# Kernel tuning notes

Measured on AMD Instinct MI355X. Metric: run time of the kernel, lower is better.

## Reference

```python
import jax, jax.numpy as jnp
import numpy as np

H, C = 8, 16          # heads, per-head dim; hidden = H*C = 128
NEG_SLOPE = 0.2       # GATConv default
EPS = 1e-5            # GraphNorm eps


def setup_inputs() -> dict:
    key = jax.random.key(0)
    ks = iter(jax.random.split(key, 64))
    Np, Na, D, E = 100000, 50000, 128, 500000
    s = 1.0 / np.sqrt(D)

    def w(shape, scale=1.0):
        return jax.random.normal(next(ks), shape, jnp.float32) * scale

    inp = {
        'x_paper': w((Np, D)),
        'x_author': w((Na, D)),
        'edge_writes': jnp.stack([
            jax.random.randint(next(ks), (E,), 0, Na),
            jax.random.randint(next(ks), (E,), 0, Np)]).astype(jnp.int32),
        'edge_cites': jnp.stack([
            jax.random.randint(next(ks), (E,), 0, Np),
            jax.random.randint(next(ks), (E,), 0, Np)]).astype(jnp.int32),
        'W_lin_paper': w((D, 128), s), 'b_lin_paper': jnp.zeros((128,), jnp.float32),
        'W_lin_author': w((D, 128), s), 'b_lin_author': jnp.zeros((128,), jnp.float32),
        'Wsrc_writes': w((128, 128), s), 'Wdst_writes': w((128, 128), s),
        'atts_writes': w((H, C), 0.1), 'attd_writes': w((H, C), 0.1),
        'bias_writes': jnp.zeros((128,), jnp.float32),
        'Wsrc_cites': w((128, 128), s), 'Wdst_cites': w((128, 128), s),
        'atts_cites': w((H, C), 0.1), 'attd_cites': w((H, C), 0.1),
        'bias_cites': jnp.zeros((128,), jnp.float32),
        'gnw_paper': jnp.ones((128,), jnp.float32), 'gnb_paper': jnp.zeros((128,), jnp.float32),
        'gnm_paper': jnp.ones((128,), jnp.float32),
        'gnw_author': jnp.ones((128,), jnp.float32), 'gnb_author': jnp.zeros((128,), jnp.float32),
        'gnm_author': jnp.ones((128,), jnp.float32),
        'W2_paper': w((128, 128), s), 'b2_paper': jnp.zeros((128,), jnp.float32),
        'W2_author': w((128, 128), s), 'b2_author': jnp.zeros((128,), jnp.float32),
    }
    return inp


def _gat(src_emb, dst_emb, ei, Wsrc, Wdst, att_s, att_d, bias, n_dst):
    # PyG GATConv, bipartite input, concat=True, add_self_loops=True (eval / no dropout)
    n_self = min(src_emb.shape[0], n_dst)
    loops = jnp.arange(n_self, dtype=ei.dtype)
    src = jnp.concatenate([ei[0], loops])
    dst = jnp.concatenate([ei[1], loops])
    xs = (src_emb @ Wsrc).reshape(-1, H, C)          # [Ns,H,C]
    xd = (dst_emb @ Wdst).reshape(-1, H, C)          # [Nd,H,C]
    a_s = (xs * att_s).sum(-1)                       # [Ns,H]
    a_d = (xd * att_d).sum(-1)                       # [Nd,H]
    e = jax.nn.leaky_relu(a_s[src] + a_d[dst], NEG_SLOPE)   # [E,H]
    m = jax.ops.segment_max(e, dst, num_segments=n_dst)
    m = jnp.where(jnp.isfinite(m), m, 0.0)           # guard empty segments
    p = jnp.exp(e - m[dst])
    denom = jax.ops.segment_sum(p, dst, num_segments=n_dst)
    alpha = p / (denom[dst] + 1e-16)                 # segment softmax over dst
    msg = xs[src] * alpha[:, :, None]                # [E,H,C]
    out = jax.ops.segment_sum(msg, dst, num_segments=n_dst)  # [Nd,H,C]
    return out.reshape(n_dst, H * C) + bias


def _gnorm(x, w, b, ms):
    mu = x.mean(0)
    o = x - ms * mu
    var = (o * o).mean(0)
    return w * o * jax.lax.rsqrt(var + EPS) + b


def reference(x_paper, x_author, edge_writes, edge_cites,
              W_lin_paper, b_lin_paper, W_lin_author, b_lin_author,
              Wsrc_writes, Wdst_writes, atts_writes, attd_writes, bias_writes,
              Wsrc_cites, Wdst_cites, atts_cites, attd_cites, bias_cites,
              gnw_paper, gnb_paper, gnm_paper, gnw_author, gnb_author, gnm_author,
              W2_paper, b2_paper, W2_author, b2_author):
    emb_p = jax.nn.relu(x_paper @ W_lin_paper + b_lin_paper)
    emb_a = jax.nn.relu(x_author @ W_lin_author + b_lin_author)
    Np = emb_p.shape[0]
    out_p = _gat(emb_a, emb_p, edge_writes, Wsrc_writes, Wdst_writes,
                 atts_writes, attd_writes, bias_writes, Np)
    out_p = out_p + _gat(emb_p, emb_p, edge_cites, Wsrc_cites, Wdst_cites,
                         atts_cites, attd_cites, bias_cites, Np)
    out_a = jnp.zeros((emb_a.shape[0], H * C), x_author.dtype)  # no edge type targets author
    out_p = _gnorm(out_p, gnw_paper, gnb_paper, gnm_paper) @ W2_paper + b2_paper
    out_a = _gnorm(out_a, gnw_author, gnb_author, gnm_author) @ W2_author + b2_author
    return (out_p, out_a)
```

## Files before the change

kernel.cpp:

```cpp
#include <hip/hip_runtime.h>
#include <cstdint>
#include <cstddef>

#define H 8
#define DHID 128
#define BM 64
#define LDST 136
#define NEG_SLOPE 0.2f
#define GN_EPS 1e-5f

#define SCAN_T 256
#define SCAN_I 4

typedef __attribute__((ext_vector_type(8))) short short8;
typedef __attribute__((ext_vector_type(4))) float f32x4;

__device__ __forceinline__ void atomAddF(float* p, float v) {
    __hip_atomic_fetch_add(p, v, __ATOMIC_RELAXED, __HIP_MEMORY_SCOPE_AGENT);
}
__device__ __forceinline__ unsigned short f2bf(float f) {
    uint32_t u = __float_as_uint(f);
    uint32_t r = (u + 0x7FFFu + ((u >> 16) & 1u)) >> 16;
    return (unsigned short)r;
}
__device__ __forceinline__ uint32_t pack2bf(float lo, float hi) {
    return (uint32_t)f2bf(lo) | ((uint32_t)f2bf(hi) << 16);
}
__device__ __forceinline__ float bflo(uint32_t v) { return __uint_as_float(v << 16); }
__device__ __forceinline__ float bfhi(uint32_t v) { return __uint_as_float(v & 0xFFFF0000u); }

struct PrepHist {
    const float *Wlp, *Wsc, *Wla, *Wsw, *W2p;
    const float *Wdw, *adw, *asc_, *Wdc, *adc_, *asw_;
    unsigned short *WlinP_p, *WsrcP_c, *WlinP_a, *WsrcP_w, *W2P_p, *VscP_p, *VscP_a;
    const float *bw, *bc, *gnb_a, *W2a, *b2a;
    float *bsum, *row_a, *colsum, *colsumsq;
    unsigned short *xs_w_ph, *xs_c_ph;
    float *as_w_ph, *as_c_ph;
    const int *dst_w, *dst_c;
    int *deg, *rank;
    int Ew, Ec, Np, HB0;
};

__global__ void prep_hist(PrepHist a) {
    int b = blockIdx.x, t = threadIdx.x;
    if (b >= a.HB0) {
        int base = (b - a.HB0) * 1024 + t;
        int E = a.Ew + a.Ec;
        int dd[4];
        bool val[4];
#pragma unroll
        for (int j = 0; j < 4; ++j) {
            int i = base + j * 256;
            val[j] = i < E;
            dd[j] = 0;
            if (val[j]) dd[j] = (i < a.Ew) ? a.dst_w[i] : (a.Np + a.dst_c[i - a.Ew]);
        }
        int rk[4];
#pragma unroll
        for (int j = 0; j < 4; ++j)
            if (val[j]) rk[j] = atomicAdd(&a.deg[dd[j]], 1);
#pragma unroll
        for (int j = 0; j < 4; ++j)
            if (val[j]) a.rank[base + j * 256] = rk[j];
        return;
    }
    if (b == 56) {
        if (t < 128) {
            a.bsum[t] = a.bw[t] + a.bc[t];
            float acc = a.b2a[t];
            for (int k = 0; k < DHID; ++k) acc += a.gnb_a[k] * a.W2a[k * DHID + t];
            a.row_a[t] = acc;
            a.colsum[t] = 0.f;
            a.colsumsq[t] = 0.f;
            a.xs_w_ph[t] = 0;
            a.xs_c_ph[t] = 0;
        } else if (t < 136) a.as_w_ph[t - 128] = -1e30f;
        else if (t < 144) a.as_c_ph[t - 136] = -1e30f;
        return;
    }
    int j = b >> 3;
    int idx = (b & 7) * 256 + t;
    int lane = idx & 63, kk = (idx >> 6) & 3, nt = idx >> 8;
    int col = nt * 16 + (lane & 15);
    int k0 = kk * 32 + ((lane >> 4) << 3);
    if (j < 5) {
        const float* W = j == 0 ? a.Wlp : j == 1 ? a.Wsc : j == 2 ? a.Wla : j == 3 ? a.Wsw : a.W2p;
        unsigned short* out = j == 0 ? a.WlinP_p : j == 1 ? a.WsrcP_c : j == 2 ? a.WlinP_a
                              : j == 3 ? a.WsrcP_w : a.W2P_p;
        for (int i = 0; i < 8; ++i) out[idx * 8 + i] = f2bf(W[(k0 + i) * DHID + col]);
    } else if (j == 5) {
        if (idx >= 2 * 256) return;
        const float *W = nullptr, *A = nullptr;
        int h = col & 7;
        if (col < 24) {
            int which = col >> 3;
            W = which == 0 ? a.Wdw : which == 1 ? a.Wsc : a.Wdc;
            A = which == 0 ? a.adw : which == 1 ? a.asc_ : a.adc_;
        }
        for (int i = 0; i < 8; ++i) {
            float v = 0.f;
            if (W)
                for (int c = 0; c < 16; ++c) v += W[(k0 + i) * DHID + h * 16 + c] * A[h * 16 + c];
            a.VscP_p[idx * 8 + i] = f2bf(v);
        }
    } else {
        if (idx >= 256) return;
        int h = col & 7;
        for (int i = 0; i < 8; ++i) {
            float v = 0.f;
            if (col < 8)
                for (int c = 0; c < 16; ++c)
                    v += a.Wsw[(k0 + i) * DHID + h * 16 + c] * a.asw_[h * 16 + c];
            a.VscP_a[idx * 8 + i] = f2bf(v);
        }
    }
}

__global__ void scan1(const int* __restrict__ in, int n, int* __restrict__ out,
                      int* __restrict__ bsums) {
    __shared__ int sh[SCAN_T];
    int t = threadIdx.x;
    long base = (long)blockIdx.x * SCAN_T * SCAN_I;
    int v[SCAN_I];
    int s = 0;
#pragma unroll
    for (int j = 0; j < SCAN_I; ++j) {
        long idx = base + (long)t * SCAN_I + j;
        int x = (idx < n) ? in[idx] : 0;
        x = (x + 3) & ~3;
        v[j] = x;
        s += x;
    }
    sh[t] = s;
    __syncthreads();
    for (int off = 1; off < SCAN_T; off <<= 1) {
        int x = (t >= off) ? sh[t - off] : 0;
        __syncthreads();
        sh[t] += x;
        __syncthreads();
    }
    int run = sh[t] - s;
#pragma unroll
    for (int j = 0; j < SCAN_I; ++j) {
        long idx = base + (long)t * SCAN_I + j;
        if (idx < n) out[idx] = run;
        run += v[j];
    }
    if (t == SCAN_T - 1) bsums[blockIdx.x] = sh[SCAN_T - 1];
}

__global__ void scan3_tails(const int* __restrict__ off_raw, const int* __restrict__ bs1,
                            int nb, int n2, int* __restrict__ off2,
                            const int* __restrict__ deg,
                            int Np, int Na, int* __restrict__ srcu) {
    __shared__ int pf[SCAN_T];
    int t = threadIdx.x;
    pf[t] = (t < nb) ? bs1[t] : 0;
    __syncthreads();
    for (int off = 1; off < SCAN_T; off <<= 1) {
        int x = (t >= off) ? pf[t - off] : 0;
        __syncthreads();
        pf[t] += x;
        __syncthreads();
    }
    int i = blockIdx.x * 256 + t;
    if (i < n2) {
        int g = i >> 10;
        int o = off_raw[i] + (g ? pf[g - 1] : 0);
        off2[i] = o;
        int dgi = deg[i];
        int padded = (dgi + 3) & ~3;
        int ph = (i < Np) ? Na : Np;
        for (int k = dgi; k < padded; ++k) srcu[o + k] = ph;
    }
    if (blockIdx.x == 0 && t == 0) off2[n2] = pf[nb - 1];
}

template <int NSC>
__device__ void proj_body(unsigned short* xt, int bid,
                          const float* __restrict__ x, int nrows,
                          const unsigned short* __restrict__ WlinP, const float* __restrict__ blin,
                          const unsigned short* __restrict__ WsrcP,
                          const unsigned short* __restrict__ VscP,
                          unsigned short* __restrict__ xs,
                          float* __restrict__ a0, float* __restrict__ a1, float* __restrict__ a2) {
    int t = threadIdx.x;
    int lane = t & 63, w = t >> 6;
    long row0 = (long)bid * BM;
    int wrow0 = w * 16;
    for (int it = 0; it < 16; ++it) {
        int r = wrow0 + it;
        long gr = row0 + r;
        float v0 = 0.f, v1 = 0.f;
        if (gr < nrows) { v0 = x[gr * DHID + 2 * lane]; v1 = x[gr * DHID + 2 * lane + 1]; }
        *reinterpret_cast<uint32_t*>(&xt[r * LDST + 2 * lane]) = pack2bf(v0, v1);
    }
    int arow = wrow0 + (lane & 15);
    int koff = (lane >> 4) << 3;
    short8 af[4];
#pragma unroll
    for (int kk = 0; kk < 4; ++kk)
        af[kk] = *reinterpret_cast<const short8*>(&xt[arow * LDST + kk * 32 + koff]);
    const short8* Bl = reinterpret_cast<const short8*>(WlinP);
    f32x4 acc[8];
#pragma unroll
    for (int nt = 0; nt < 8; ++nt) {
        f32x4 a = {0.f, 0.f, 0.f, 0.f};
#pragma unroll
        for (int kk = 0; kk < 4; ++kk)
            a = __builtin_amdgcn_mfma_f32_16x16x32_bf16(af[kk], Bl[(nt * 4 + kk) * 64 + lane], a, 0, 0, 0);
        acc[nt] = a;
    }
    int orow = wrow0 + ((lane >> 4) << 2);
    int ccol = lane & 15;
#pragma unroll
    for (int nt = 0; nt < 8; ++nt) {
        float b = blin[nt * 16 + ccol];
#pragma unroll
        for (int r = 0; r < 4; ++r) {
            float e = fmaxf(acc[nt][r] + b, 0.f);
            xt[(orow + r) * LDST + nt * 16 + ccol] = f2bf(e);
        }
    }
#pragma unroll
    for (int kk = 0; kk < 4; ++kk)
        af[kk] = *reinterpret_cast<const short8*>(&xt[arow * LDST + kk * 32 + koff]);
    const short8* Bs = reinterpret_cast<const short8*>(WsrcP);
#pragma unroll
    for (int nt = 0; nt < 8; ++nt) {
        f32x4 a = {0.f, 0.f, 0.f, 0.f};
#pragma unroll
        for (int kk = 0; kk < 4; ++kk)
            a = __builtin_amdgcn_mfma_f32_16x16x32_bf16(af[kk], Bs[(nt * 4 + kk) * 64 + lane], a, 0, 0, 0);
        acc[nt] = a;
    }
    const short8* Bv = reinterpret_cast<const short8*>(VscP);
    f32x4 sacc0 = {0.f, 0.f, 0.f, 0.f}, sacc1 = {0.f, 0.f, 0.f, 0.f};
#pragma unroll
    for (int kk = 0; kk < 4; ++kk)
        sacc0 = __builtin_amdgcn_mfma_f32_16x16x32_bf16(af[kk], Bv[kk * 64 + lane], sacc0, 0, 0, 0);
    if (NSC > 1) {
#pragma unroll
        for (int kk = 0; kk < 4; ++kk)
            sacc1 = __builtin_amdgcn_mfma_f32_16x16x32_bf16(af[kk], Bv[(4 + kk) * 64 + lane], sacc1, 0, 0, 0);
    }
#pragma unroll
    for (int nt = 0; nt < 8; ++nt) {
#pragma unroll
        for (int r = 0; r < 4; ++r) {
            long gr = row0 + orow + r;
            if (gr < nrows) xs[gr * DHID + nt * 16 + ccol] = f2bf(acc[nt][r]);
        }
    }
#pragma unroll
    for (int st = 0; st < NSC; ++st) {
        int scol = st * 16 + ccol;
        int h = scol & 7, which = scol >> 3;
        float* ap = which == 0 ? a0 : which == 1 ? a1 : which == 2 ? a2 : nullptr;
        if (ap) {
            f32x4 s = st == 0 ? sacc0 : sacc1;
#pragma unroll
            for (int r = 0; r < 4; ++r) {
                long gr = row0 + orow + r;
                if (gr < nrows) ap[gr * H + h] = s[r];
            }
        }
    }
}

struct MegaArgs {
    const float* x_p; int Np;
    const unsigned short* WlinP_p; const float* blp;
    const unsigned short* WsrcP_c; const unsigned short* VscP_p;
    unsigned short* xs_c; float *a_d_w, *a_s_c, *a_d_c;
    const float* x_a; int Na;
    const unsigned short* WlinP_a; const float* bla;
    const unsigned short* WsrcP_w; const unsigned short* VscP_a;
    unsigned short* xs_w; float* a_s_w;
    const int *src_w, *dst_w, *src_c, *dst_c;
    int Ew, Ec;
    const int *off2, *rank;
    int* srcu;
    int PB, AB;
};

__global__ __launch_bounds__(256) void mega(MegaArgs a) {
    __shared__ unsigned short xt[BM * LDST];
    int b = blockIdx.x;
    if (b < a.PB) {
        proj_body<2>(xt, b, a.x_p, a.Np, a.WlinP_p, a.blp, a.WsrcP_c, a.VscP_p,
                     a.xs_c, a.a_d_w, a.a_s_c, a.a_d_c);
        return;
    }
    if (b < a.PB + a.AB) {
        proj_body<1>(xt, b - a.PB, a.x_a, a.Na, a.WlinP_a, a.bla, a.WsrcP_w, a.VscP_a,
                     a.xs_w, a.a_s_w, nullptr, nullptr);
        return;
    }
    int base = (b - a.PB - a.AB) * 1024 + threadIdx.x;
    int E = a.Ew + a.Ec;
    int s[4], di[4], rk[4];
    bool val[4];
#pragma unroll
    for (int j = 0; j < 4; ++j) {
        int i = base + j * 256;
        val[j] = i < E;
        s[j] = di[j] = rk[j] = 0;
        if (val[j]) {
            if (i < a.Ew) { s[j] = a.src_w[i]; di[j] = a.dst_w[i]; }
            else { int q = i - a.Ew; s[j] = a.src_c[q]; di[j] = a.Np + a.dst_c[q]; }
            rk[j] = a.rank[i];
        }
    }
    int pos[4];
#pragma unroll
    for (int j = 0; j < 4; ++j)
        if (val[j]) pos[j] = a.off2[di[j]] + rk[j];
#pragma unroll
    for (int j = 0; j < 4; ++j)
        if (val[j]) a.srcu[pos[j]] = s[j];
}

#define FILLB 391
__global__ __launch_bounds__(256) void gat_gather(
    const int* __restrict__ off, const int* __restrict__ srcu,
    const float* __restrict__ a_s_w, const float* __restrict__ a_d_w,
    const float* __restrict__ a_s_c, const float* __restrict__ a_d_c,
    const unsigned short* __restrict__ xs_w, const unsigned short* __restrict__ xs_c,
    uint32_t* __restrict__ gatb, int Np, int nselfw,
    const float* __restrict__ row_a, float4* __restrict__ outa, long n4) {
    if (blockIdx.x < FILLB) {
        long i = (long)blockIdx.x * 256 + threadIdx.x;
        long stride = (long)FILLB * 256;
        const float4* r4 = reinterpret_cast<const float4*>(row_a);
        for (; i < n4; i += stride) outa[i] = r4[i & 31];
        return;
    }
    int l = threadIdx.x & 63;
    int d = (blockIdx.x - FILLB) * 4 + (threadIdx.x >> 6);
    if (d >= Np) return;
    int h = l >> 3;
    int iw = off[d], w1 = off[d + 1];
    int ic = off[Np + d], c1 = off[Np + d + 1];
    float adw = a_d_w[(long)d * H + h];
    float adc = a_d_c[(long)d * H + h];
    float denw = 0.f, n0w = 0.f, n1w = 0.f;
    float denc = 0.f, n0c = 0.f, n1c = 0.f;
    if (d < nselfw) {
        float e = a_s_w[(long)d * H + h] + adw;
        e = e > 0.f ? e : NEG_SLOPE * e;
        float p = __expf(e);
        uint32_t v = *reinterpret_cast<const uint32_t*>(xs_w + (long)d * DHID + 2 * l);
        denw += p; n0w += p * bflo(v); n1w += p * bfhi(v);
    }
    {
        float e = a_s_c[(long)d * H + h] + adc;
        e = e > 0.f ? e : NEG_SLOPE * e;
        float p = __expf(e);
        uint32_t v = *reinterpret_cast<const uint32_t*>(xs_c + (long)d * DHID + 2 * l);
        denc += p; n0c += p * bflo(v); n1c += p * bfhi(v);
    }
    while (iw < w1 || ic < c1) {
        bool hw = iw < w1, hc = ic < c1;
        int4 sw, sc;
        if (hw) sw = *reinterpret_cast<const int4*>(srcu + iw);
        if (hc) sc = *reinterpret_cast<const int4*>(srcu + ic);
        float ew[4], ec[4];
        uint32_t vw[4], vc[4];
        if (hw) {
            ew[0] = a_s_w[(long)sw.x * H + h];
            ew[1] = a_s_w[(long)sw.y * H + h];
            ew[2] = a_s_w[(long)sw.z * H + h];
            ew[3] = a_s_w[(long)sw.w * H + h];
            vw[0] = *reinterpret_cast<const uint32_t*>(xs_w + (long)sw.x * DHID + 2 * l);
            vw[1] = *reinterpret_cast<const uint32_t*>(xs_w + (long)sw.y * DHID + 2 * l);
            vw[2] = *reinterpret_cast<const uint32_t*>(xs_w + (long)sw.z * DHID + 2 * l);
            vw[3] = *reinterpret_cast<const uint32_t*>(xs_w + (long)sw.w * DHID + 2 * l);
        }
        if (hc) {
            ec[0] = a_s_c[(long)sc.x * H + h];
            ec[1] = a_s_c[(long)sc.y * H + h];
            ec[2] = a_s_c[(long)sc.z * H + h];
            ec[3] = a_s_c[(long)sc.w * H + h];
            vc[0] = *reinterpret_cast<const uint32_t*>(xs_c + (long)sc.x * DHID + 2 * l);
            vc[1] = *reinterpret_cast<const uint32_t*>(xs_c + (long)sc.y * DHID + 2 * l);
            vc[2] = *reinterpret_cast<const uint32_t*>(xs_c + (long)sc.z * DHID + 2 * l);
            vc[3] = *reinterpret_cast<const uint32_t*>(xs_c + (long)sc.w * DHID + 2 * l);
        }
        if (hw) {
#pragma unroll
            for (int j = 0; j < 4; ++j) {
                float e = ew[j] + adw;
                e = e > 0.f ? e : NEG_SLOPE * e;
                float p = __expf(e);
                denw += p;
                n0w += p * bflo(vw[j]);
                n1w += p * bfhi(vw[j]);
            }
            iw += 4;
        }
        if (hc) {
#pragma unroll
            for (int j = 0; j < 4; ++j) {
                float e = ec[j] + adc;
                e = e > 0.f ? e : NEG_SLOPE * e;
                float p = __expf(e);
                denc += p;
                n0c += p * bflo(vc[j]);
                n1c += p * bfhi(vc[j]);
            }
            ic += 4;
        }
    }
    float rw = 1.f / (denw + 1e-16f);
    float rc = 1.f / (denc + 1e-16f);
    gatb[(long)d * 64 + l] = pack2bf(n0w * rw + n0c * rc, n1w * rw + n1c * rc);
}

#define GN_ROWS 512
__global__ void gn_reduce(const uint32_t* __restrict__ gatb, const float* __restrict__ bsum,
                          float* __restrict__ colsum, float* __restrict__ colsumsq, int Np) {
    int t = threadIdx.x;
    int p = t & 63, ro = t >> 6;
    long r0 = (long)blockIdx.x * GN_ROWS + ro;
    long r1 = min((long)(blockIdx.x + 1) * GN_ROWS, (long)Np);
    float b0 = bsum[2 * p], b1 = bsum[2 * p + 1];
    float s1a = 0.f, s2a = 0.f, s1b = 0.f, s2b = 0.f;
    for (long r = r0; r < r1; r += 4) {
        uint32_t u = gatb[r * 64 + p];
        float x0 = bflo(u) + b0, x1 = bfhi(u) + b1;
        s1a += x0; s2a += x0 * x0;
        s1b += x1; s2b += x1 * x1;
    }
    atomAddF(colsum + 2 * p, s1a);
    atomAddF(colsumsq + 2 * p, s2a);
    atomAddF(colsum + 2 * p + 1, s1b);
    atomAddF(colsumsq + 2 * p + 1, s2b);
}

__global__ __launch_bounds__(256) void final_fill(
    const uint32_t* __restrict__ gatb, const float* __restrict__ bsum,
    const float* __restrict__ colsum, const float* __restrict__ colsumsq,
    const float* __restrict__ gnw, const float* __restrict__ gnb,
    const float* __restrict__ gnm,
    const unsigned short* __restrict__ W2P, const float* __restrict__ b2,
    float* __restrict__ out, int Np) {
    __shared__ unsigned short xt[BM * LDST];
    __shared__ float cscale[DHID], cshift[DHID];
    int b = blockIdx.x;
    int t = threadIdx.x;
    int lane = t & 63, w = t >> 6;
    long row0 = (long)b * BM;
    if (t < DHID) {
        float invN = 1.f / (float)Np;
        float mu = colsum[t] * invN;
        float ms = gnm[t];
        float var = colsumsq[t] * invN - mu * mu * ms * (2.f - ms);
        float sc = gnw[t] * rsqrtf(var + GN_EPS);
        cscale[t] = sc;
        cshift[t] = (bsum[t] - ms * mu) * sc + gnb[t];
    }
    __syncthreads();
    int wrow0 = w * 16;
    float cs0 = cscale[2 * lane], cf0 = cshift[2 * lane];
    float cs1 = cscale[2 * lane + 1], cf1 = cshift[2 * lane + 1];
    for (int it = 0; it < 16; ++it) {
        int r = wrow0 + it;
        long gr = row0 + r;
        float v0 = 0.f, v1 = 0.f;
        if (gr < Np) {
            uint32_t u = gatb[gr * 64 + lane];
            v0 = bflo(u) * cs0 + cf0;
            v1 = bfhi(u) * cs1 + cf1;
        }
        *reinterpret_cast<uint32_t*>(&xt[r * LDST + 2 * lane]) = pack2bf(v0, v1);
    }
    int arow = wrow0 + (lane & 15);
    int koff = (lane >> 4) << 3;
    short8 af[4];
#pragma unroll
    for (int kk = 0; kk < 4; ++kk)
        af[kk] = *reinterpret_cast<const short8*>(&xt[arow * LDST + kk * 32 + koff]);
    const short8* Bw = reinterpret_cast<const short8*>(W2P);
    int orow = wrow0 + ((lane >> 4) << 2);
    int ccol = lane & 15;
#pragma unroll
    for (int nt = 0; nt < 8; ++nt) {
        f32x4 a = {0.f, 0.f, 0.f, 0.f};
#pragma unroll
        for (int kk = 0; kk < 4; ++kk)
            a = __builtin_amdgcn_mfma_f32_16x16x32_bf16(af[kk], Bw[(nt * 4 + kk) * 64 + lane], a, 0, 0, 0);
        float bb = b2[nt * 16 + ccol];
#pragma unroll
        for (int r = 0; r < 4; ++r) {
            long gr = row0 + orow + r;
            if (gr < Np) out[gr * DHID + nt * 16 + ccol] = a[r] + bb;
        }
    }
}

extern "C" void kernel_launch(void* const* d_in, const int* in_sizes, int n_in,
                              void* d_out, int out_size, void* d_ws, size_t ws_size,
                              hipStream_t stream) {
    const float* x_p   = (const float*)d_in[0];
    const float* x_a   = (const float*)d_in[1];
    const int*   e_w   = (const int*)d_in[2];
    const int*   e_c   = (const int*)d_in[3];
    const float* Wlp   = (const float*)d_in[4];
    const float* blp   = (const float*)d_in[5];
    const float* Wla   = (const float*)d_in[6];
    const float* bla   = (const float*)d_in[7];
    const float* Wsw   = (const float*)d_in[8];
    const float* Wdw   = (const float*)d_in[9];
    const float* asw   = (const float*)d_in[10];
    const float* adw   = (const float*)d_in[11];
    const float* bw    = (const float*)d_in[12];
    const float* Wsc   = (const float*)d_in[13];
    const float* Wdc   = (const float*)d_in[14];
    const float* asc   = (const float*)d_in[15];
    const float* adc   = (const float*)d_in[16];
    const float* bc    = (const float*)d_in[17];
    const float* gnw_p = (const float*)d_in[18];
    const float* gnb_p = (const float*)d_in[19];
    const float* gnm_p = (const float*)d_in[20];
    const float* gnb_a = (const float*)d_in[22];
    const float* W2p   = (const float*)d_in[24];
    const float* b2p   = (const float*)d_in[25];
    const float* W2a   = (const float*)d_in[26];
    const float* b2a   = (const float*)d_in[27];

    int Np = in_sizes[0] / DHID;
    int Na = in_sizes[1] / DHID;
    int Ew = in_sizes[2] / 2;
    int Ec = in_sizes[3] / 2;
    int nself_w = Na < Np ? Na : Np;
    int tot_edges = Ew + Ec;
    int maxTot = tot_edges + 6 * Np + 8;

    float* ws = (float*)d_ws;
    uint32_t* gatb = (uint32_t*)ws;
    float* a_d_w = (float*)(gatb + (size_t)Np * 64);
    float* a_d_c = a_d_w + (size_t)Np * H;
    float* a_s_w = a_d_c + (size_t)Np * H;
    float* a_s_c = a_s_w + (size_t)(Na + 1) * H;
    float* bsum  = a_s_c + (size_t)(Np + 1) * H;
    float* row_a = bsum + DHID;
    float* colsum   = row_a + DHID;
    float* colsumsq = colsum + DHID;
    int*   deg   = (int*)(colsumsq + DHID);
    int* off_raw = deg + 2 * Np;
    int* off2    = off_raw + 2 * Np;
    int* bs1     = off2 + 2 * Np + 1;
    uintptr_t up = (uintptr_t)(bs1 + 512);
    up = (up + 15) & ~(uintptr_t)15;
    int* srcu = (int*)up;
    int* rank = srcu + maxTot;
    unsigned short* xs_w = (unsigned short*)(rank + tot_edges);
    unsigned short* xs_c = xs_w + (size_t)(Na + 1) * DHID;
    up = (uintptr_t)(xs_c + (size_t)(Np + 1) * DHID);
    up = (up + 15) & ~(uintptr_t)15;
    unsigned short* WlinP_p = (unsigned short*)up;
    unsigned short* WsrcP_c = WlinP_p + 16384;
    unsigned short* WlinP_a = WsrcP_c + 16384;
    unsigned short* WsrcP_w = WlinP_a + 16384;
    unsigned short* W2P_p   = WsrcP_w + 16384;
    unsigned short* VscP_p  = W2P_p + 16384;
    unsigned short* VscP_a  = VscP_p + 4096;

    hipMemsetAsync(deg, 0, 2 * (size_t)Np * sizeof(int), stream);

    int HB = (tot_edges + 1023) / 1024;
    {
        PrepHist pa;
        pa.Wlp = Wlp; pa.Wsc = Wsc; pa.Wla = Wla; pa.Wsw = Wsw; pa.W2p = W2p;
        pa.Wdw = Wdw; pa.adw = adw; pa.asc_ = asc; pa.Wdc = Wdc; pa.adc_ = adc; pa.asw_ = asw;
        pa.WlinP_p = WlinP_p; pa.WsrcP_c = WsrcP_c; pa.WlinP_a = WlinP_a;
        pa.WsrcP_w = WsrcP_w; pa.W2P_p = W2P_p; pa.VscP_p = VscP_p; pa.VscP_a = VscP_a;
        pa.bw = bw; pa.bc = bc; pa.gnb_a = gnb_a; pa.W2a = W2a; pa.b2a = b2a;
        pa.bsum = bsum; pa.row_a = row_a; pa.colsum = colsum; pa.colsumsq = colsumsq;
        pa.xs_w_ph = xs_w + (size_t)Na * DHID;
        pa.xs_c_ph = xs_c + (size_t)Np * DHID;
        pa.as_w_ph = a_s_w + (size_t)Na * H;
        pa.as_c_ph = a_s_c + (size_t)Np * H;
        pa.dst_w = e_w + Ew; pa.dst_c = e_c + Ec;
        pa.deg = deg; pa.rank = rank;
        pa.Ew = Ew; pa.Ec = Ec;
        pa.Np = Np; pa.HB0 = 57;
        prep_hist<<<57 + HB, 256, 0, stream>>>(pa);
    }

    int n2 = 2 * Np;
    int nb = (n2 + SCAN_T * SCAN_I - 1) / (SCAN_T * SCAN_I);
    scan1<<<nb, SCAN_T, 0, stream>>>(deg, n2, off_raw, bs1);

    scan3_tails<<<(n2 + 255) / 256, 256, 0, stream>>>(
        off_raw, bs1, nb, n2, off2, deg, Np, Na, srcu);

    {
        MegaArgs ma;
        ma.x_p = x_p; ma.Np = Np; ma.WlinP_p = WlinP_p; ma.blp = blp;
        ma.WsrcP_c = WsrcP_c; ma.VscP_p = VscP_p;
        ma.xs_c = xs_c; ma.a_d_w = a_d_w; ma.a_s_c = a_s_c; ma.a_d_c = a_d_c;
        ma.x_a = x_a; ma.Na = Na; ma.WlinP_a = WlinP_a; ma.bla = bla;
        ma.WsrcP_w = WsrcP_w; ma.VscP_a = VscP_a;
        ma.xs_w = xs_w; ma.a_s_w = a_s_w;
        ma.src_w = e_w; ma.dst_w = e_w + Ew; ma.src_c = e_c; ma.dst_c = e_c + Ec;
        ma.Ew = Ew; ma.Ec = Ec;
        ma.off2 = off2; ma.rank = rank; ma.srcu = srcu;
        ma.PB = (Np + BM - 1) / BM;
        ma.AB = (Na + BM - 1) / BM;
        int SB = (tot_edges + 1023) / 1024;
        mega<<<ma.PB + ma.AB + SB, 256, 0, stream>>>(ma);
    }

    {
        long n4 = (long)Na * DHID / 4;
        gat_gather<<<FILLB + (Np + 3) / 4, 256, 0, stream>>>(
            off2, srcu, a_s_w, a_d_w, a_s_c, a_d_c, xs_w, xs_c, gatb, Np, nself_w,
            row_a, (float4*)((float*)d_out + (size_t)Np * DHID), n4);
    }

    gn_reduce<<<(Np + GN_ROWS - 1) / GN_ROWS, 256, 0, stream>>>(gatb, bsum, colsum, colsumsq, Np);

    final_fill<<<(Np + BM - 1) / BM, 256, 0, stream>>>(
        gatb, bsum, colsum, colsumsq, gnw_p, gnb_p, gnm_p, W2P_p, b2p,
        (float*)d_out, Np);
}
```

Measured before the change: 297.3 us.

## Interleave source attention scores into bf16 feature rows for gather locality

Source attention logits (a_s) are now stored as 8 floats appended to each projected bf16 feature row (stride 144 instead of 128), so the edge gather fetches score and features from one row instead of two separate arrays. The projection's input staging is changed to a block-cooperative coalesced load with barriers added between stages. This cuts scattered memory transactions per edge in the gather, at the cost of wider rows and extra block synchronisation in the projection.

```diff
diff --git a/kernel.cpp b/kernel.cpp
--- a/kernel.cpp
+++ b/kernel.cpp
@@ -4,6 +4,7 @@
 
 #define H 8
 #define DHID 128
+#define XST 144
 #define BM 64
 #define LDST 136
 #define NEG_SLOPE 0.2f
@@ -36,7 +37,6 @@
     const float *bw, *bc, *gnb_a, *W2a, *b2a;
     float *bsum, *row_a, *colsum, *colsumsq;
     unsigned short *xs_w_ph, *xs_c_ph;
-    float *as_w_ph, *as_c_ph;
     const int *dst_w, *dst_c;
     int *deg, *rank;
     int Ew, Ec, Np, HB0;
@@ -75,8 +75,11 @@
             a.colsumsq[t] = 0.f;
             a.xs_w_ph[t] = 0;
             a.xs_c_ph[t] = 0;
-        } else if (t < 136) a.as_w_ph[t - 128] = -1e30f;
-        else if (t < 144) a.as_c_ph[t - 136] = -1e30f;
+        } else if (t < 136) {
+            *reinterpret_cast<float*>(a.xs_w_ph + 128 + 2 * (t - 128)) = -1e30f;
+        } else if (t < 144) {
+            *reinterpret_cast<float*>(a.xs_c_ph + 128 + 2 * (t - 136)) = -1e30f;
+        }
         return;
     }
     int j = b >> 3;
@@ -184,19 +187,20 @@
                           const unsigned short* __restrict__ WsrcP,
                           const unsigned short* __restrict__ VscP,
                           unsigned short* __restrict__ xs,
-                          float* __restrict__ a0, float* __restrict__ a1, float* __restrict__ a2) {
+                          float* __restrict__ ad0, float* __restrict__ ad1) {
     int t = threadIdx.x;
     int lane = t & 63, w = t >> 6;
     long row0 = (long)bid * BM;
-    int wrow0 = w * 16;
     for (int it = 0; it < 16; ++it) {
-        int r = wrow0 + it;
+        int idx2 = t + it * 256;
+        int r = idx2 >> 6, cp = idx2 & 63;
         long gr = row0 + r;
         float v0 = 0.f, v1 = 0.f;
-        if (gr < nrows) { v0 = x[gr * DHID + 2 * lane]; v1 = x[gr * DHID + 2 * lane + 1]; }
-        *reinterpret_cast<uint32_t*>(&xt[r * LDST + 2 * lane]) = pack2bf(v0, v1);
-    }
-    int arow = wrow0 + (lane & 15);
+        if (gr < nrows) { v0 = x[gr * DHID + 2 * cp]; v1 = x[gr * DHID + 2 * cp + 1]; }
+        *reinterpret_cast<uint32_t*>(&xt[r * LDST + 2 * cp]) = pack2bf(v0, v1);
+    }
+    __syncthreads();
+    int arow = w * 16 + (lane & 15);
     int koff = (lane >> 4) << 3;
     short8 af[4];
 #pragma unroll
@@ -212,7 +216,8 @@
             a = __builtin_amdgcn_mfma_f32_16x16x32_bf16(af[kk], Bl[(nt * 4 + kk) * 64 + lane], a, 0, 0, 0);
         acc[nt] = a;
     }
-    int orow = wrow0 + ((lane >> 4) << 2);
+    __syncthreads();
+    int orow = w * 16 + ((lane >> 4) << 2);
     int ccol = lane & 15;
 #pragma unroll
     for (int nt = 0; nt < 8; ++nt) {
@@ -223,6 +228,7 @@
             xt[(orow + r) * LDST + nt * 16 + ccol] = f2bf(e);
         }
     }
+    __syncthreads();
 #pragma unroll
     for (int kk = 0; kk < 4; ++kk)
         af[kk] = *reinterpret_cast<const short8*>(&xt[arow * LDST + kk * 32 + koff]);
@@ -250,20 +256,26 @@
 #pragma unroll
         for (int r = 0; r < 4; ++r) {
             long gr = row0 + orow + r;
-            if (gr < nrows) xs[gr * DHID + nt * 16 + ccol] = f2bf(acc[nt][r]);
+            if (gr < nrows) xs[gr * XST + nt * 16 + ccol] = f2bf(acc[nt][r]);
         }
     }
 #pragma unroll
     for (int st = 0; st < NSC; ++st) {
         int scol = st * 16 + ccol;
         int h = scol & 7, which = scol >> 3;
-        float* ap = which == 0 ? a0 : which == 1 ? a1 : which == 2 ? a2 : nullptr;
-        if (ap) {
-            f32x4 s = st == 0 ? sacc0 : sacc1;
-#pragma unroll
-            for (int r = 0; r < 4; ++r) {
-                long gr = row0 + orow + r;
-                if (gr < nrows) ap[gr * H + h] = s[r];
+        f32x4 s = (st == 0) ? sacc0 : sacc1;
+#pragma unroll
+        for (int r = 0; r < 4; ++r) {
+            long gr = row0 + orow + r;
+            if (gr >= nrows) continue;
+            if (NSC == 2) {
+                if (which == 0) ad0[gr * H + h] = s[r];
+                else if (which == 1)
+                    *reinterpret_cast<float*>(xs + gr * XST + 128 + 2 * h) = s[r];
+                else if (which == 2) ad1[gr * H + h] = s[r];
+            } else {
+                if (which == 0)
+                    *reinterpret_cast<float*>(xs + gr * XST + 128 + 2 * h) = s[r];
             }
         }
     }
@@ -273,11 +285,11 @@
     const float* x_p; int Np;
     const unsigned short* WlinP_p; const float* blp;
     const unsigned short* WsrcP_c; const unsigned short* VscP_p;
-    unsigned short* xs_c; float *a_d_w, *a_s_c, *a_d_c;
+    unsigned short* xs_c; float *a_d_w, *a_d_c;
     const float* x_a; int Na;
     const unsigned short* WlinP_a; const float* bla;
     const unsigned short* WsrcP_w; const unsigned short* VscP_a;
-    unsigned short* xs_w; float* a_s_w;
+    unsigned short* xs_w;
     const int *src_w, *dst_w, *src_c, *dst_c;
     int Ew, Ec;
     const int *off2, *rank;
@@ -290,12 +302,12 @@
     int b = blockIdx.x;
     if (b < a.PB) {
         proj_body<2>(xt, b, a.x_p, a.Np, a.WlinP_p, a.blp, a.WsrcP_c, a.VscP_p,
-                     a.xs_c, a.a_d_w, a.a_s_c, a.a_d_c);
+                     a.xs_c, a.a_d_w, a.a_d_c);
         return;
     }
     if (b < a.PB + a.AB) {
         proj_body<1>(xt, b - a.PB, a.x_a, a.Na, a.WlinP_a, a.bla, a.WsrcP_w, a.VscP_a,
-                     a.xs_w, a.a_s_w, nullptr, nullptr);
+                     a.xs_w, nullptr, nullptr);
         return;
     }
     int base = (b - a.PB - a.AB) * 1024 + threadIdx.x;
@@ -325,8 +337,7 @@
 #define FILLB 391
 __global__ __launch_bounds__(256) void gat_gather(
     const int* __restrict__ off, const int* __restrict__ srcu,
-    const float* __restrict__ a_s_w, const float* __restrict__ a_d_w,
-    const float* __restrict__ a_s_c, const float* __restrict__ a_d_c,
+    const float* __restrict__ a_d_w, const float* __restrict__ a_d_c,
     const unsigned short* __restrict__ xs_w, const unsigned short* __restrict__ xs_c,
     uint32_t* __restrict__ gatb, int Np, int nselfw,
     const float* __restrict__ row_a, float4* __restrict__ outa, long n4) {
@@ -341,6 +352,7 @@
     int d = (blockIdx.x - FILLB) * 4 + (threadIdx.x >> 6);
     if (d >= Np) return;
     int h = l >> 3;
+    int sco = 128 + 2 * h;
     int iw = off[d], w1 = off[d + 1];
     int ic = off[Np + d], c1 = off[Np + d + 1];
     float adw = a_d_w[(long)d * H + h];
@@ -348,17 +360,19 @@
     float denw = 0.f, n0w = 0.f, n1w = 0.f;
     float denc = 0.f, n0c = 0.f, n1c = 0.f;
     if (d < nselfw) {
-        float e = a_s_w[(long)d * H + h] + adw;
+        const unsigned short* r = xs_w + (long)d * XST;
+        float e = *reinterpret_cast<const float*>(r + sco) + adw;
         e = e > 0.f ? e : NEG_SLOPE * e;
         float p = __expf(e);
-        uint32_t v = *reinterpret_cast<const uint32_t*>(xs_w + (long)d * DHID + 2 * l);
+        uint32_t v = *reinterpret_cast<const uint32_t*>(r + 2 * l);
         denw += p; n0w += p * bflo(v); n1w += p * bfhi(v);
     }
     {
-        float e = a_s_c[(long)d * H + h] + adc;
+        const unsigned short* r = xs_c + (long)d * XST;
+        float e = *reinterpret_cast<const float*>(r + sco) + adc;
         e = e > 0.f ? e : NEG_SLOPE * e;
         float p = __expf(e);
-        uint32_t v = *reinterpret_cast<const uint32_t*>(xs_c + (long)d * DHID + 2 * l);
+        uint32_t v = *reinterpret_cast<const uint32_t*>(r + 2 * l);
         denc += p; n0c += p * bflo(v); n1c += p * bfhi(v);
     }
     while (iw < w1 || ic < c1) {
@@ -369,24 +383,32 @@
         float ew[4], ec[4];
         uint32_t vw[4], vc[4];
         if (hw) {
-            ew[0] = a_s_w[(long)sw.x * H + h];
-            ew[1] = a_s_w[(long)sw.y * H + h];
-            ew[2] = a_s_w[(long)sw.z * H + h];
-            ew[3] = a_s_w[(long)sw.w * H + h];
-            vw[0] = *reinterpret_cast<const uint32_t*>(xs_w + (long)sw.x * DHID + 2 * l);
-            vw[1] = *reinterpret_cast<const uint32_t*>(xs_w + (long)sw.y * DHID + 2 * l);
-            vw[2] = *reinterpret_cast<const uint32_t*>(xs_w + (long)sw.z * DHID + 2 * l);
-            vw[3] = *reinterpret_cast<const uint32_t*>(xs_w + (long)sw.w * DHID + 2 * l);
+            const unsigned short* r0 = xs_w + (long)sw.x * XST;
+            const unsigned short* r1 = xs_w + (long)sw.y * XST;
+            const unsigned short* r2 = xs_w + (long)sw.z * XST;
+            const unsigned short* r3 = xs_w + (long)sw.w * XST;
+            ew[0] = *reinterpret_cast<const float*>(r0 + sco);
+            ew[1] = *reinterpret_cast<const float*>(r1 + sco);
+            ew[2] = *reinterpret_cast<const float*>(r2 + sco);
+            ew[3] = *reinterpret_cast<const float*>(r3 + sco);
+            vw[0] = *reinterpret_cast<const uint32_t*>(r0 + 2 * l);
+            vw[1] = *reinterpret_cast<const uint32_t*>(r1 + 2 * l);
+            vw[2] = *reinterpret_cast<const uint32_t*>(r2 + 2 * l);
+            vw[3] = *reinterpret_cast<const uint32_t*>(r3 + 2 * l);
         }
         if (hc) {
-            ec[0] = a_s_c[(long)sc.x * H + h];
-            ec[1] = a_s_c[(long)sc.y * H + h];
-            ec[2] = a_s_c[(long)sc.z * H + h];
-            ec[3] = a_s_c[(long)sc.w * H + h];
-            vc[0] = *reinterpret_cast<const uint32_t*>(xs_c + (long)sc.x * DHID + 2 * l);
-            vc[1] = *reinterpret_cast<const uint32_t*>(xs_c + (long)sc.y * DHID + 2 * l);
-            vc[2] = *reinterpret_cast<const uint32_t*>(xs_c + (long)sc.z * DHID + 2 * l);
-            vc[3] = *reinterpret_cast<const uint32_t*>(xs_c + (long)sc.w * DHID + 2 * l);
+            const unsigned short* r0 = xs_c + (long)sc.x * XST;
+            const unsigned short* r1 = xs_c + (long)sc.y * XST;
+            const unsigned short* r2 = xs_c + (long)sc.z * XST;
+            const unsigned short* r3 = xs_c + (long)sc.w * XST;
+            ec[0] = *reinterpret_cast<const float*>(r0 + sco);
+            ec[1] = *reinterpret_cast<const float*>(r1 + sco);
+            ec[2] = *reinterpret_cast<const float*>(r2 + sco);
+            ec[3] = *reinterpret_cast<const float*>(r3 + sco);
+            vc[0] = *reinterpret_cast<const uint32_t*>(r0 + 2 * l);
+            vc[1] = *reinterpret_cast<const uint32_t*>(r1 + 2 * l);
+            vc[2] = *reinterpret_cast<const uint32_t*>(r2 + 2 * l);
+            vc[3] = *reinterpret_cast<const uint32_t*>(r3 + 2 * l);
         }
         if (hw) {
 #pragma unroll
@@ -542,9 +564,7 @@
     uint32_t* gatb = (uint32_t*)ws;
     float* a_d_w = (float*)(gatb + (size_t)Np * 64);
     float* a_d_c = a_d_w + (size_t)Np * H;
-    float* a_s_w = a_d_c + (size_t)Np * H;
-    float* a_s_c = a_s_w + (size_t)(Na + 1) * H;
-    float* bsum  = a_s_c + (size_t)(Np + 1) * H;
+    float* bsum  = a_d_c + (size_t)Np * H;
     float* row_a = bsum + DHID;
     float* colsum   = row_a + DHID;
     float* colsumsq = colsum + DHID;
@@ -557,8 +577,8 @@
     int* srcu = (int*)up;
     int* rank = srcu + maxTot;
     unsigned short* xs_w = (unsigned short*)(rank + tot_edges);
-    unsigned short* xs_c = xs_w + (size_t)(Na + 1) * DHID;
-    up = (uintptr_t)(xs_c + (size_t)(Np + 1) * DHID);
+    unsigned short* xs_c = xs_w + (size_t)(Na + 1) * XST;
+    up = (uintptr_t)(xs_c + (size_t)(Np + 1) * XST);
     up = (up + 15) & ~(uintptr_t)15;
     unsigned short* WlinP_p = (unsigned short*)up;
     unsigned short* WsrcP_c = WlinP_p + 16384;
@@ -579,10 +599,8 @@
         pa.WsrcP_w = WsrcP_w; pa.W2P_p = W2P_p; pa.VscP_p = VscP_p; pa.VscP_a = VscP_a;
         pa.bw = bw; pa.bc = bc; pa.gnb_a = gnb_a; pa.W2a = W2a; pa.b2a = b2a;
         pa.bsum = bsum; pa.row_a = row_a; pa.colsum = colsum; pa.colsumsq = colsumsq;
-        pa.xs_w_ph = xs_w + (size_t)Na * DHID;
-        pa.xs_c_ph = xs_c + (size_t)Np * DHID;
-        pa.as_w_ph = a_s_w + (size_t)Na * H;
-        pa.as_c_ph = a_s_c + (size_t)Np * H;
+        pa.xs_w_ph = xs_w + (size_t)Na * XST;
+        pa.xs_c_ph = xs_c + (size_t)Np * XST;
         pa.dst_w = e_w + Ew; pa.dst_c = e_c + Ec;
         pa.deg = deg; pa.rank = rank;
         pa.Ew = Ew; pa.Ec = Ec;
@@ -601,10 +619,10 @@
         MegaArgs ma;
         ma.x_p = x_p; ma.Np = Np; ma.WlinP_p = WlinP_p; ma.blp = blp;
         ma.WsrcP_c = WsrcP_c; ma.VscP_p = VscP_p;
-        ma.xs_c = xs_c; ma.a_d_w = a_d_w; ma.a_s_c = a_s_c; ma.a_d_c = a_d_c;
+        ma.xs_c = xs_c; ma.a_d_w = a_d_w; ma.a_d_c = a_d_c;
         ma.x_a = x_a; ma.Na = Na; ma.WlinP_a = WlinP_a; ma.bla = bla;
         ma.WsrcP_w = WsrcP_w; ma.VscP_a = VscP_a;
-        ma.xs_w = xs_w; ma.a_s_w = a_s_w;
+        ma.xs_w = xs_w;
         ma.src_w = e_w; ma.dst_w = e_w + Ew; ma.src_c = e_c; ma.dst_c = e_c + Ec;
         ma.Ew = Ew; ma.Ec = Ec;
         ma.off2 = off2; ma.rank = rank; ma.srcu = srcu;
@@ -617,7 +635,7 @@
     {
         long n4 = (long)Na * DHID / 4;
         gat_gather<<<FILLB + (Np + 3) / 4, 256, 0, stream>>>(
-            off2, srcu, a_s_w, a_d_w, a_s_c, a_d_c, xs_w, xs_c, gatb, Np, nself_w,
+            off2, srcu, a_d_w, a_d_c, xs_w, xs_c, gatb, Np, nself_w,
             row_a, (float4*)((float*)d_out + (size_t)Np * DHID), n4);
     }
 
```

Result: faster. 281.8 us (-5.2%).
